# Kernel optimization log

Hardware: AMD Instinct MI355X
Metric: run time of the kernel (lower is better)

## Reference

```python
import jax, jax.numpy as jnp
import numpy as np

DIM = 512
HEADS = 8
HEAD_DIM = DIM // HEADS // 2  # 32
KS = 7  # kernel_size
DIL = 1


def _window_and_pb_start(length, ks):
    nh = ks // 2
    i = jnp.arange(length)
    ni = jnp.clip(i - nh, 0, length - ks)                       # neighborhood start
    pi = nh + jnp.maximum(nh - i, 0) + jnp.where(i + nh >= length, length - i - 1 - nh, 0)
    return ni, pi


def na_attention(qkv_na, rpb):
    # qkv_na: [B,H,W,3*heads*hd]
    B, H, W, _ = qkv_na.shape
    qkv = qkv_na.reshape(B, H, W, 3, HEADS, HEAD_DIM)
    qkv = jnp.transpose(qkv, (3, 0, 4, 1, 2, 5))                 # [3,B,h,H,W,d]
    q, k, v = qkv[0], qkv[1], qkv[2]
    scale = HEAD_DIM ** -0.5
    ni, pi = _window_and_pb_start(H, KS)
    nj, pj = _window_and_pb_start(W, KS)
    off = jnp.arange(KS)
    idx_i = ni[:, None] + off[None, :]                           # [H,K]
    idx_j = nj[:, None] + off[None, :]                           # [W,K]
    # gather neighborhoods: [B,h,H,W,K,K,d]
    kn = k[:, :, idx_i[:, None, :, None], idx_j[None, :, None, :], :]
    vn = v[:, :, idx_i[:, None, :, None], idx_j[None, :, None, :], :]
    bias_i = pi[:, None] + off[None, :]                          # [H,K]
    bias_j = pj[:, None] + off[None, :]                          # [W,K]
    bias = rpb[:, bias_i[:, None, :, None], bias_j[None, :, None, :]]  # [h,H,W,K,K]
    attn = jnp.einsum('bhijd,bhijkld->bhijkl', q * scale, kn) + bias[None]
    a = attn.reshape(B, HEADS, H, W, KS * KS)
    a = jax.nn.softmax(a, axis=-1).reshape(B, HEADS, H, W, KS, KS)
    out = jnp.einsum('bhijkl,bhijkld->bhijd', a, vn)             # [B,h,H,W,d]
    return jnp.transpose(out, (0, 2, 3, 1, 4)).reshape(B, H, W, HEADS * HEAD_DIM)


def self_attention(qkv_self):
    # qkv_self: [B,H,W,3*heads*hd]
    B, H, W, _ = qkv_self.shape
    N = H * W
    qkv = qkv_self.reshape(B, N, 3, HEADS, HEAD_DIM)
    qkv = jnp.transpose(qkv, (2, 0, 3, 1, 4))                    # [3,B,h,N,d]
    q, k, v = qkv[0], qkv[1], qkv[2]
    scale = HEAD_DIM ** -0.5
    scores = jnp.einsum('bhnd,bhmd->bhnm', q * scale, k)
    a = jax.nn.softmax(scores, axis=-1)
    out = jnp.einsum('bhnm,bhmd->bhnd', a, v)
    out = jnp.transpose(out, (0, 2, 1, 3)).reshape(B, H, W, HEADS * HEAD_DIM)
    return out


def setup_inputs() -> dict:
    key = jax.random.key(0)
    ks = jax.random.split(key, 6)
    B, H, W = 2, 48, 48
    x = jax.random.normal(ks[0], (B, H, W, DIM), dtype=jnp.float32)
    W_qkv = jax.random.normal(ks[1], (DIM, 3 * DIM), dtype=jnp.float32) * (DIM ** -0.5)
    b_qkv = jax.random.normal(ks[2], (3 * DIM,), dtype=jnp.float32) * 0.02
    rpb = jax.random.normal(ks[3], (HEADS, 2 * KS - 1, 2 * KS - 1), dtype=jnp.float32) * 0.02
    W_proj = jax.random.normal(ks[4], (DIM, DIM), dtype=jnp.float32) * (DIM ** -0.5)
    b_proj = jax.random.normal(ks[5], (DIM,), dtype=jnp.float32) * 0.02
    return {"x": x, "W_qkv": W_qkv, "b_qkv": b_qkv, "rpb": rpb, "W_proj": W_proj, "b_proj": b_proj}


def reference(x, W_qkv, b_qkv, rpb, W_proj, b_proj):
    B, H, W, C = x.shape
    qkv = x @ W_qkv + b_qkv                                      # [B,H,W,3C]
    qkv_na, qkv_self = qkv[..., : 3 * C // 2], qkv[..., 3 * C // 2:]
    x_na = na_attention(qkv_na, rpb)                             # [B,H,W,C//2]
    x_self = self_attention(qkv_self)                            # [B,H,W,C//2]
    out = jnp.concatenate([x_na, x_self], axis=-1) @ W_proj + b_proj
    return out
```

## Files before the change

kernel.cpp:

```cpp
#include <hip/hip_runtime.h>
#include <cstdint>
#include <cstddef>


#define DIMC 512
#define HEADS 8
#define HD 32
#define KSZ 7
#define HH 48
#define WW 48
#define BB 2
#define NPIX (HH * WW)
#define ROWS (BB * NPIX)
#define C3 (3 * DIMC)
#define TK 64
#define KSPLIT 4
#define KCHUNK (NPIX / KSPLIT)
#define NTILES (KCHUNK / TK)
#define QB 128
#define NQBLK (NPIX / QB)
#define NFLASH (16 * NQBLK * KSPLIT)
#define ROWE 40
#define VSTR 72
#define VROWE 232
#define LOG2E 1.4426950408889634f

typedef __attribute__((ext_vector_type(8))) short short8;
typedef __attribute__((ext_vector_type(4))) float f32x4;
union frag8 { short8 s; uint32_t u[4]; };

static __device__ __forceinline__ float bf2f(uint32_t u) {
    return __builtin_bit_cast(float, u << 16);
}
static __device__ __forceinline__ uint16_t f2bf(float f) {
    uint32_t x = __builtin_bit_cast(uint32_t, f);
    uint32_t r = x + 0x7fffu + ((x >> 16) & 1u);
    return (uint16_t)(r >> 16);
}
static __device__ __forceinline__ uint32_t cvtpk(float lo, float hi) {
    uint32_t r;
    asm("v_cvt_pk_bf16_f32 %0, %1, %2" : "=v"(r) : "v"(lo), "v"(hi));
    return r;
}
static __device__ __forceinline__ float ex2(float x) {
    return __builtin_amdgcn_exp2f(x);
}

__global__ __launch_bounds__(256)
void prep_weights(const float* __restrict__ Wqkv, const float* __restrict__ Wproj,
                  uint16_t* __restrict__ wqt, uint16_t* __restrict__ wpt)
{
    __shared__ float tile[32][33];
    int bid = blockIdx.x;
    const float* W; uint16_t* Wt; int N;
    if (bid < 768) { W = Wqkv; Wt = wqt; N = C3; }
    else { bid -= 768; W = Wproj; Wt = wpt; N = DIMC; }
    const int kt = bid & 15, nt = bid >> 4;
    const int K = DIMC;
    const int tx = threadIdx.x & 31, ty = threadIdx.x >> 5;
    const int k0 = kt * 32, n0 = nt * 32;
    #pragma unroll
    for (int i = 0; i < 4; ++i)
        tile[ty + 8 * i][tx] = W[(size_t)(k0 + ty + 8 * i) * N + n0 + tx];
    __syncthreads();
    #pragma unroll
    for (int i = 0; i < 4; ++i)
        Wt[(size_t)(n0 + ty + 8 * i) * K + k0 + tx] = f2bf(tile[tx][ty + 8 * i]);
}

template<bool A_F32, bool OUT_F32, bool QSCALE>
__global__ __launch_bounds__(256)
void gemm_mfma(const void* __restrict__ Av, const uint16_t* __restrict__ Bt,
               const float* __restrict__ bias, void* __restrict__ Cv,
               int M, int N, int K)
{
    constexpr int BM = 128, BK = 32;
    constexpr float QSC = 0.17677669529663687f * LOG2E;
    __shared__ __align__(16) uint16_t Al[BM * ROWE];
    __shared__ __align__(16) uint16_t Bl[BM * ROWE];
    const int tid = threadIdx.x;
    const int lane = tid & 63, wv = tid >> 6;
    const int c = lane & 15, g = lane >> 4;
    const int wr = wv >> 1, wc = wv & 1;
    const int m0 = blockIdx.y * BM, n0 = blockIdx.x * BM;
    const int srow = tid >> 2, skc = (tid & 3) * 8;

    f32x4 acc[4][4];
    #pragma unroll
    for (int mi = 0; mi < 4; ++mi)
        #pragma unroll
        for (int ni = 0; ni < 4; ++ni)
            acc[mi][ni] = (f32x4){0.f, 0.f, 0.f, 0.f};

    for (int k0 = 0; k0 < K; k0 += BK) {
        __syncthreads();
        #pragma unroll
        for (int half = 0; half < 2; ++half) {
            const int row = srow + half * 64;
            if (A_F32) {
                const float* A32 = (const float*)Av;
                const float4 a0 = *reinterpret_cast<const float4*>(&A32[(size_t)(m0 + row) * K + k0 + skc]);
                const float4 a1 = *reinterpret_cast<const float4*>(&A32[(size_t)(m0 + row) * K + k0 + skc + 4]);
                *reinterpret_cast<uint4*>(&Al[row * ROWE + skc]) =
                    make_uint4(cvtpk(a0.x, a0.y), cvtpk(a0.z, a0.w),
                               cvtpk(a1.x, a1.y), cvtpk(a1.z, a1.w));
            } else {
                const uint16_t* A16 = (const uint16_t*)Av;
                *reinterpret_cast<uint4*>(&Al[row * ROWE + skc]) =
                    *reinterpret_cast<const uint4*>(&A16[(size_t)(m0 + row) * K + k0 + skc]);
            }
            *reinterpret_cast<uint4*>(&Bl[row * ROWE + skc]) =
                *reinterpret_cast<const uint4*>(&Bt[(size_t)(n0 + row) * K + k0 + skc]);
        }
        __syncthreads();

        frag8 a[4], b[4];
        #pragma unroll
        for (int mi = 0; mi < 4; ++mi)
            a[mi].s = *reinterpret_cast<const short8*>(&Al[(wr * 64 + mi * 16 + c) * ROWE + g * 8]);
        #pragma unroll
        for (int ni = 0; ni < 4; ++ni)
            b[ni].s = *reinterpret_cast<const short8*>(&Bl[(wc * 64 + ni * 16 + c) * ROWE + g * 8]);
        #pragma unroll
        for (int mi = 0; mi < 4; ++mi)
            #pragma unroll
            for (int ni = 0; ni < 4; ++ni)
                acc[mi][ni] = __builtin_amdgcn_mfma_f32_16x16x32_bf16(
                    a[mi].s, b[ni].s, acc[mi][ni], 0, 0, 0);
    }

    #pragma unroll
    for (int mi = 0; mi < 4; ++mi) {
        #pragma unroll
        for (int ni = 0; ni < 4; ++ni) {
            const int row = m0 + wr * 64 + mi * 16 + 4 * g;
            const int col = n0 + wc * 64 + ni * 16 + c;
            const float bv = bias[col];
            float f = 1.f;
            if (QSCALE) f = (col < 256 || (col >= 768 && col < 1024)) ? QSC : 1.f;
            #pragma unroll
            for (int r = 0; r < 4; ++r) {
                const float val = (acc[mi][ni][r] + bv) * f;
                if (OUT_F32)
                    ((float*)Cv)[(size_t)(row + r) * N + col] = val;
                else
                    ((uint16_t*)Cv)[(size_t)(row + r) * N + col] = f2bf(val);
            }
        }
    }
}

static __device__ __forceinline__
void na_body(uint8_t* smem, int bid, const uint16_t* __restrict__ qkv,
             const float* __restrict__ rpb, uint16_t* __restrict__ attn)
{
    uint16_t* K_l   = (uint16_t*)smem;
    uint16_t* Vt    = (uint16_t*)(smem + 17920);
    float*    rpb_l = (float*)(smem + 32768);

    const int tid = threadIdx.x;
    const int lane = tid & 63, wv = tid >> 6;
    const int c = lane & 15, g = lane >> 4, g4 = g * 4;
    const int tile = bid % 36;
    const int bh = bid / 36;
    const int h = bh & (HEADS - 1), b = bh >> 3;
    const int t0i = (tile / 6) * 8, t0j = (tile % 6) * 8;
    const int u0i = min(max(t0i - 3, 0), HH - 14);
    const int u0j = min(max(t0j - 3, 0), WW - 14);
    const size_t rowbase = (size_t)b * NPIX;

    if (tid < 169) rpb_l[tid] = rpb[h * 169 + tid] * LOG2E;
    #pragma unroll
    for (int it = 0; it < 4; ++it) {
        const int idx = it * 256 + tid;
        if (idx < 896) {
            const int u = idx >> 2, dc = idx & 3;
            const int uc = u & 15, ur = u >> 4;
            if (uc < 14) {
                const int grow = (u0i + ur) * WW + (u0j + uc);
                const uint16_t* src = qkv + (rowbase + grow) * C3 + 256 + h * HD + dc * 8;
                *reinterpret_cast<uint4*>(&K_l[u * ROWE + dc * 8]) =
                    *reinterpret_cast<const uint4*>(src);
                const uint4 vw = *reinterpret_cast<const uint4*>(src + 256);
                const uint16_t* vh = reinterpret_cast<const uint16_t*>(&vw);
                #pragma unroll
                for (int i = 0; i < 8; ++i)
                    Vt[(dc * 8 + i) * VROWE + u] = vh[i];
            } else {
                *reinterpret_cast<uint4*>(&K_l[u * ROWE + dc * 8]) = make_uint4(0, 0, 0, 0);
                #pragma unroll
                for (int i = 0; i < 8; ++i)
                    Vt[(dc * 8 + i) * VROWE + u] = 0;
            }
        }
    }

    const int qid = wv * 16 + c;
    const int qi = t0i + (qid >> 3), qj = t0j + (qid & 7);
    const int pixq = qi * WW + qj;
    const int niq = min(max(qi - 3, 0), HH - KSZ);
    const int njq = min(max(qj - 3, 0), WW - KSZ);
    const int piq = 3 + max(3 - qi, 0) + ((qi + 3 >= HH) ? (HH - qi - 4) : 0);
    const int pjq = 3 + max(3 - qj, 0) + ((qj + 3 >= WW) ? (WW - qj - 4) : 0);
    const int ni_rel = niq - u0i, nj_rel = njq - u0j;
    const int bb = (piq - ni_rel) * 13 + (pjq - nj_rel);

    frag8 qf;
    qf.s = *reinterpret_cast<const short8*>(qkv + (rowbase + pixq) * C3 + h * HD + g * 8);

    __syncthreads();

    float pex[14][4];
    float m = -1e30f;
    #pragma unroll
    for (int f = 0; f < 14; ++f) {
        frag8 ka;
        ka.s = *reinterpret_cast<const short8*>(&K_l[(16 * f + c) * ROWE + g * 8]);
        f32x4 s = {0.f, 0.f, 0.f, 0.f};
        s = __builtin_amdgcn_mfma_f32_16x16x32_bf16(ka.s, qf.s, s, 0, 0, 0);
        const bool rok = (unsigned)(f - ni_rel) < 7u;
        #pragma unroll
        for (int r = 0; r < 4; ++r) {
            const int uc = g4 + r;
            const bool ok = rok && ((unsigned)(uc - nj_rel) < 7u);
            const int addr = ok ? (bb + 13 * f + uc) : 0;
            const float v = s[r] + rpb_l[addr];
            pex[f][r] = ok ? v : -1e30f;
            m = fmaxf(m, pex[f][r]);
        }
    }
    m = fmaxf(m, __shfl_xor(m, 16));
    m = fmaxf(m, __shfl_xor(m, 32));
    float l = 0.f;
    #pragma unroll
    for (int f = 0; f < 14; ++f)
        #pragma unroll
        for (int r = 0; r < 4; ++r) {
            pex[f][r] = ex2(pex[f][r] - m);
            l += pex[f][r];
        }
    l += __shfl_xor(l, 16);
    l += __shfl_xor(l, 32);

    f32x4 of0 = {0.f, 0.f, 0.f, 0.f}, of1 = {0.f, 0.f, 0.f, 0.f};
    const int sbase = (g & 1) * 32 + c;
    #pragma unroll
    for (int kk = 0; kk < 7; ++kk) {
        uint32_t pk0[2], pk1[2];
        pk0[0] = cvtpk(pex[2 * kk][0], pex[2 * kk][1]);
        pk0[1] = cvtpk(pex[2 * kk][2], pex[2 * kk][3]);
        pk1[0] = cvtpk(pex[2 * kk + 1][0], pex[2 * kk + 1][1]);
        pk1[1] = cvtpk(pex[2 * kk + 1][2], pex[2 * kk + 1][3]);
        frag8 pb;
        #pragma unroll
        for (int tt = 0; tt < 4; ++tt) {
            const int srcLane = sbase + ((tt >> 1) << 4);
            const uint32_t v0 = __shfl(pk0[tt & 1], srcLane);
            const uint32_t v1 = __shfl(pk1[tt & 1], srcLane);
            pb.u[tt] = (g >= 2) ? v1 : v0;
        }
        frag8 va0, va1;
        va0.s = *reinterpret_cast<const short8*>(&Vt[c * VROWE + kk * 32 + g * 8]);
        va1.s = *reinterpret_cast<const short8*>(&Vt[(16 + c) * VROWE + kk * 32 + g * 8]);
        of0 = __builtin_amdgcn_mfma_f32_16x16x32_bf16(va0.s, pb.s, of0, 0, 0, 0);
        of1 = __builtin_amdgcn_mfma_f32_16x16x32_bf16(va1.s, pb.s, of1, 0, 0, 0);
    }

    const float invl = 1.f / l;
    uint32_t* dst = reinterpret_cast<uint32_t*>(attn + (rowbase + pixq) * DIMC + h * HD);
    dst[2 * g + 0] = cvtpk(of0[0] * invl, of0[1] * invl);
    dst[2 * g + 1] = cvtpk(of0[2] * invl, of0[3] * invl);
    dst[8 + 2 * g + 0] = cvtpk(of1[0] * invl, of1[1] * invl);
    dst[8 + 2 * g + 1] = cvtpk(of1[2] * invl, of1[3] * invl);
}

static __device__ __forceinline__
void flash_body(uint8_t* smem, int bid, const uint16_t* __restrict__ qkv,
                uint16_t* __restrict__ po, float2* __restrict__ pml)
{
    uint16_t (*Ks)[TK * ROWE]  = (uint16_t (*)[TK * ROWE])smem;
    uint16_t (*Vt)[32 * VSTR]  = (uint16_t (*)[32 * VSTR])(smem + 10240);

    const int tid = threadIdx.x;
    const int lane = tid & 63, wv = tid >> 6;
    const int c = lane & 15, g = lane >> 4;
    const int split = bid & (KSPLIT - 1);
    const int qblk = (bid >> 2) % NQBLK;
    const int bh = bid / (KSPLIT * NQBLK);
    const int h = bh & (HEADS - 1);
    const int b = bh >> 3;
    const size_t rowbase = (size_t)b * NPIX;
    const int qbase = qblk * QB + wv * 32;
    const int q0 = qbase + c, q1 = qbase + 16 + c;

    frag8 qf0, qf1;
    qf0.s = *reinterpret_cast<const short8*>(qkv + (rowbase + q0) * C3 + 768 + h * HD + g * 8);
    qf1.s = *reinterpret_cast<const short8*>(qkv + (rowbase + q1) * C3 + 768 + h * HD + g * 8);

    float m0 = -1e30f, m1 = -1e30f, ls0 = 0.f, ls1 = 0.f;
    f32x4 oa00 = {0,0,0,0}, oa01 = {0,0,0,0};
    f32x4 oa10 = {0,0,0,0}, oa11 = {0,0,0,0};

    const int skk = tid >> 2, kd = (tid & 3) * 8;
    const int sgk = (skk & 15) | ((skk & 16) << 1) | ((skk & 32) >> 1);
    const int skv = tid >> 3, sdc = tid & 7;
    const int cp2 = 2 * (skv ^ ((sdc >> 1) << 3));

    uint4 KW; uint2 VA, VB;
#define STAGE_LOAD(T) do {                                                            \
    const size_t _tb = rowbase + split * KCHUNK + (T) * TK;                           \
    KW = *reinterpret_cast<const uint4*>(qkv + (_tb + sgk) * C3 + 1024 + h * HD + kd);\
    const uint16_t* _vp = qkv + (_tb + skv) * C3 + 1280 + h * HD + sdc * 4;           \
    VA = *reinterpret_cast<const uint2*>(_vp);                                        \
    VB = *reinterpret_cast<const uint2*>(_vp + 32 * C3); } while (0)

#define STAGE_WRITE(BUF) do {                                                         \
    *reinterpret_cast<uint4*>(&Ks[BUF][skk * ROWE + kd]) = KW;                        \
    const uint32_t _pa[4] = {VA.x & 0xffffu, VA.x >> 16, VA.y & 0xffffu, VA.y >> 16}; \
    const uint32_t _pb[4] = {VB.x & 0xffffu, VB.x >> 16, VB.y & 0xffffu, VB.y >> 16}; \
    _Pragma("unroll")                                                                 \
    for (int _i = 0; _i < 4; ++_i)                                                    \
        *reinterpret_cast<uint32_t*>(&Vt[BUF][(sdc * 4 + _i) * VSTR + cp2]) =         \
            _pa[_i] | (_pb[_i] << 16); } while (0)

    STAGE_LOAD(0);
    STAGE_WRITE(0);

    const int x0 = (c >> 3) << 3;
    const int x1 = 16 + x0;

    for (int t = 0; t < NTILES; ++t) {
        __syncthreads();

        const bool more = (t + 1 < NTILES);
        if (more) STAGE_LOAD(t + 1);

        const int cur = t & 1;
        frag8 ka0, ka1, ka2, ka3;
        ka0.s = *reinterpret_cast<const short8*>(&Ks[cur][c * ROWE + g * 8]);
        ka1.s = *reinterpret_cast<const short8*>(&Ks[cur][(16 + c) * ROWE + g * 8]);
        ka2.s = *reinterpret_cast<const short8*>(&Ks[cur][(32 + c) * ROWE + g * 8]);
        ka3.s = *reinterpret_cast<const short8*>(&Ks[cur][(48 + c) * ROWE + g * 8]);
        f32x4 sc0[4], sc1[4];
        #pragma unroll
        for (int kf = 0; kf < 4; ++kf) {
            sc0[kf] = (f32x4){0,0,0,0};
            sc1[kf] = (f32x4){0,0,0,0};
        }
        __builtin_amdgcn_s_setprio(1);
        sc0[0] = __builtin_amdgcn_mfma_f32_16x16x32_bf16(ka0.s, qf0.s, sc0[0], 0, 0, 0);
        sc0[1] = __builtin_amdgcn_mfma_f32_16x16x32_bf16(ka1.s, qf0.s, sc0[1], 0, 0, 0);
        sc0[2] = __builtin_amdgcn_mfma_f32_16x16x32_bf16(ka2.s, qf0.s, sc0[2], 0, 0, 0);
        sc0[3] = __builtin_amdgcn_mfma_f32_16x16x32_bf16(ka3.s, qf0.s, sc0[3], 0, 0, 0);
        sc1[0] = __builtin_amdgcn_mfma_f32_16x16x32_bf16(ka0.s, qf1.s, sc1[0], 0, 0, 0);
        sc1[1] = __builtin_amdgcn_mfma_f32_16x16x32_bf16(ka1.s, qf1.s, sc1[1], 0, 0, 0);
        sc1[2] = __builtin_amdgcn_mfma_f32_16x16x32_bf16(ka2.s, qf1.s, sc1[2], 0, 0, 0);
        sc1[3] = __builtin_amdgcn_mfma_f32_16x16x32_bf16(ka3.s, qf1.s, sc1[3], 0, 0, 0);
        __builtin_amdgcn_s_setprio(0);

        float t0 = sc0[0][0], t1 = sc1[0][0];
        #pragma unroll
        for (int kf = 0; kf < 4; ++kf)
            #pragma unroll
            for (int r = 0; r < 4; ++r) {
                t0 = fmaxf(t0, sc0[kf][r]);
                t1 = fmaxf(t1, sc1[kf][r]);
            }
        t0 = fmaxf(t0, __shfl_xor(t0, 16)); t0 = fmaxf(t0, __shfl_xor(t0, 32));
        t1 = fmaxf(t1, __shfl_xor(t1, 16)); t1 = fmaxf(t1, __shfl_xor(t1, 32));

        const int ok = (t0 - m0 <= 11.54f) && (t1 - m1 <= 11.54f);
        if (!__all(ok)) {
            const float nm0 = fmaxf(m0, t0), nm1 = fmaxf(m1, t1);
            const float c0 = ex2(m0 - nm0), c1 = ex2(m1 - nm1);
            ls0 *= c0; ls1 *= c1;
            oa00 *= c0; oa01 *= c0; oa10 *= c1; oa11 *= c1;
            m0 = nm0; m1 = nm1;
        }

        #pragma unroll
        for (int kf = 0; kf < 4; ++kf)
            #pragma unroll
            for (int r = 0; r < 4; ++r) {
                sc0[kf][r] = ex2(sc0[kf][r] - m0); ls0 += sc0[kf][r];
                sc1[kf][r] = ex2(sc1[kf][r] - m1); ls1 += sc1[kf][r];
            }

        #pragma unroll
        for (int kk = 0; kk < 2; ++kk) {
            frag8 pb0, pb1;
            #pragma unroll
            for (int tt = 0; tt < 4; ++tt) {
                pb0.u[tt] = cvtpk(sc0[2 * kk][tt], sc0[2 * kk + 1][tt]);
                pb1.u[tt] = cvtpk(sc1[2 * kk][tt], sc1[2 * kk + 1][tt]);
            }
            const int p0 = 16 * kk + 4 * g;
            frag8 va0, va1;
            va0.s = *reinterpret_cast<const short8*>(&Vt[cur][c * VSTR + 2 * (p0 ^ x0)]);
            va1.s = *reinterpret_cast<const short8*>(&Vt[cur][(16 + c) * VSTR + 2 * (p0 ^ x1)]);
            __builtin_amdgcn_s_setprio(1);
            oa00 = __builtin_amdgcn_mfma_f32_16x16x32_bf16(va0.s, pb0.s, oa00, 0, 0, 0);
            oa01 = __builtin_amdgcn_mfma_f32_16x16x32_bf16(va1.s, pb0.s, oa01, 0, 0, 0);
            oa10 = __builtin_amdgcn_mfma_f32_16x16x32_bf16(va0.s, pb1.s, oa10, 0, 0, 0);
            oa11 = __builtin_amdgcn_mfma_f32_16x16x32_bf16(va1.s, pb1.s, oa11, 0, 0, 0);
            __builtin_amdgcn_s_setprio(0);
        }

        if (more) STAGE_WRITE(cur ^ 1);
    }

    ls0 += __shfl_xor(ls0, 16); ls0 += __shfl_xor(ls0, 32);
    ls1 += __shfl_xor(ls1, 16); ls1 += __shfl_xor(ls1, 32);

    const float i0 = 1.f / ls0, i1 = 1.f / ls1;
    const size_t item0 = ((size_t)split * 16 + bh) * NPIX + q0;
    const size_t item1 = ((size_t)split * 16 + bh) * NPIX + q1;
    uint32_t* d0 = reinterpret_cast<uint32_t*>(po + item0 * HD);
    d0[2 * g + 0] = cvtpk(oa00[0] * i0, oa00[1] * i0);
    d0[2 * g + 1] = cvtpk(oa00[2] * i0, oa00[3] * i0);
    d0[8 + 2 * g + 0] = cvtpk(oa01[0] * i0, oa01[1] * i0);
    d0[8 + 2 * g + 1] = cvtpk(oa01[2] * i0, oa01[3] * i0);
    uint32_t* d1 = reinterpret_cast<uint32_t*>(po + item1 * HD);
    d1[2 * g + 0] = cvtpk(oa10[0] * i1, oa10[1] * i1);
    d1[2 * g + 1] = cvtpk(oa10[2] * i1, oa10[3] * i1);
    d1[8 + 2 * g + 0] = cvtpk(oa11[0] * i1, oa11[1] * i1);
    d1[8 + 2 * g + 1] = cvtpk(oa11[2] * i1, oa11[3] * i1);
    if (g == 0) {
        pml[item0] = make_float2(m0, ls0);
        pml[item1] = make_float2(m1, ls1);
    }
#undef STAGE_LOAD
#undef STAGE_WRITE
}

__global__ __launch_bounds__(256)
void attn_fused(const uint16_t* __restrict__ qkv, const float* __restrict__ rpb,
                uint16_t* __restrict__ attn, uint16_t* __restrict__ po,
                float2* __restrict__ pml)
{
    __shared__ __align__(16) uint8_t smem[33456];
    const int bid = blockIdx.x;
    if (bid < NFLASH)
        flash_body(smem, bid, qkv, po, pml);
    else
        na_body(smem, bid - NFLASH, qkv, rpb, attn);
}

__global__ __launch_bounds__(256)
void self_attn_combine(const uint16_t* __restrict__ po, const float2* __restrict__ pml,
                       uint16_t* __restrict__ attn)
{
    const int idx = blockIdx.x * 256 + threadIdx.x;
    const int d = idx & (HD - 1);
    const int q = (idx >> 5) % NPIX;
    const int bh = idx / (HD * NPIX);
    const int h = bh & (HEADS - 1);
    const int b = bh >> 3;

    float2 ml[KSPLIT];
    float M = -1e30f;
    #pragma unroll
    for (int s = 0; s < KSPLIT; ++s) {
        ml[s] = pml[((size_t)s * 16 + bh) * NPIX + q];
        M = fmaxf(M, ml[s].x);
    }
    float num = 0.f, den = 0.f;
    #pragma unroll
    for (int s = 0; s < KSPLIT; ++s) {
        const float w = ex2(ml[s].x - M) * ml[s].y;
        const float o = bf2f((uint32_t)po[(((size_t)s * 16 + bh) * NPIX + q) * HD + d]);
        num = fmaf(w, o, num);
        den += w;
    }
    attn[((size_t)b * NPIX + q) * DIMC + 256 + h * HD + d] = f2bf(num / den);
}

extern "C" void kernel_launch(void* const* d_in, const int* in_sizes, int n_in,
                              void* d_out, int out_size, void* d_ws, size_t ws_size,
                              hipStream_t stream)
{
    const float* x     = (const float*)d_in[0];
    const float* Wqkv  = (const float*)d_in[1];
    const float* bqkv  = (const float*)d_in[2];
    const float* rpb   = (const float*)d_in[3];
    const float* Wproj = (const float*)d_in[4];
    const float* bproj = (const float*)d_in[5];

    uint16_t* qkv  = (uint16_t*)d_ws;
    uint16_t* attn = qkv + (size_t)ROWS * C3;
    uint16_t* wqt  = attn + (size_t)ROWS * DIMC;
    uint16_t* wpt  = wqt + (size_t)C3 * DIMC;
    uint16_t* po   = wpt + (size_t)DIMC * DIMC;
    float2*   pml  = (float2*)(po + (size_t)KSPLIT * 16 * NPIX * HD);

    const dim3 blk(256);
    prep_weights<<<dim3(1024), blk, 0, stream>>>(Wqkv, Wproj, wqt, wpt);
    gemm_mfma<true, false, true><<<dim3(C3 / 128, ROWS / 128), blk, 0, stream>>>(
        x, wqt, bqkv, qkv, ROWS, C3, DIMC);
    attn_fused<<<dim3(NFLASH + BB * HEADS * 36), blk, 0, stream>>>(qkv, rpb, attn, po, pml);
    self_attn_combine<<<dim3((16 * NPIX * HD) / 256), blk, 0, stream>>>(po, pml, attn);
    gemm_mfma<false, true, false><<<dim3(DIMC / 128, ROWS / 128), blk, 0, stream>>>(
        attn, wpt, bproj, d_out, ROWS, DIMC, DIMC);
}
```

Baseline: 81.90 us.

## Fuse split-K flash combine into attention kernel via last-block atomic counter

Removes the separate self_attn_combine launch. Each flash split block now bumps a per-(head, query-block) atomic counter after writing its partial output and max/sum. The last split to arrive merges all KSPLIT partials and writes the final bf16 self-attention output, then resets the counter. This saves a kernel launch and a pass over global memory, at the cost of threadfences, an atomic per block, and a serial merge tail in whichever block finishes last.

```diff
diff --git a/kernel.cpp b/kernel.cpp
--- a/kernel.cpp
+++ b/kernel.cpp
@@ -20,10 +20,13 @@
 #define QB 128
 #define NQBLK (NPIX / QB)
 #define NFLASH (16 * NQBLK * KSPLIT)
+#define NNA (BB * HEADS * 36)
+#define NGRP (16 * NQBLK)
 #define ROWE 40
 #define VSTR 72
 #define VROWE 232
 #define LOG2E 1.4426950408889634f
+#define SMEM_BYTES 33456
 
 typedef __attribute__((ext_vector_type(8))) short short8;
 typedef __attribute__((ext_vector_type(4))) float f32x4;
@@ -48,10 +51,14 @@
 
 __global__ __launch_bounds__(256)
 void prep_weights(const float* __restrict__ Wqkv, const float* __restrict__ Wproj,
-                  uint16_t* __restrict__ wqt, uint16_t* __restrict__ wpt)
+                  uint16_t* __restrict__ wqt, uint16_t* __restrict__ wpt,
+                  int* __restrict__ cnt)
 {
     __shared__ float tile[32][33];
     int bid = blockIdx.x;
+    if (bid == 0) {
+        for (int i = threadIdx.x; i < NGRP; i += 256) cnt[i] = 0;
+    }
     const float* W; uint16_t* Wt; int N;
     if (bid < 768) { W = Wqkv; Wt = wqt; N = C3; }
     else { bid -= 768; W = Wproj; Wt = wpt; N = DIMC; }
@@ -276,7 +283,8 @@
 
 static __device__ __forceinline__
 void flash_body(uint8_t* smem, int bid, const uint16_t* __restrict__ qkv,
-                uint16_t* __restrict__ po, float2* __restrict__ pml)
+                uint16_t* __restrict__ po, float2* __restrict__ pml,
+                uint16_t* __restrict__ attn, int* __restrict__ cnt)
 {
     uint16_t (*Ks)[TK * ROWE]  = (uint16_t (*)[TK * ROWE])smem;
     uint16_t (*Vt)[32 * VSTR]  = (uint16_t (*)[32 * VSTR])(smem + 10240);
@@ -429,6 +437,61 @@
         pml[item0] = make_float2(m0, ls0);
         pml[item1] = make_float2(m1, ls1);
     }
+
+    __syncthreads();
+    volatile int* flag = (volatile int*)smem;
+    __threadfence();
+    if (tid == 0) {
+        const int grp = bh * NQBLK + qblk;
+        *flag = atomicAdd(&cnt[grp], 1);
+    }
+    __syncthreads();
+    if (*flag == KSPLIT - 1) {
+        __threadfence();
+        const int ql = tid >> 1;
+        const int d0c = (tid & 1) * 16;
+        const int q = qblk * QB + ql;
+        float2 mlv[KSPLIT];
+        float M2 = -1e30f;
+        #pragma unroll
+        for (int s = 0; s < KSPLIT; ++s) {
+            mlv[s] = pml[((size_t)(s * 16 + bh)) * NPIX + q];
+            M2 = fmaxf(M2, mlv[s].x);
+        }
+        float ws_[KSPLIT], den = 0.f;
+        #pragma unroll
+        for (int s = 0; s < KSPLIT; ++s) {
+            ws_[s] = ex2(mlv[s].x - M2) * mlv[s].y;
+            den += ws_[s];
+        }
+        const float inv = 1.f / den;
+        float accv[16] = {};
+        #pragma unroll
+        for (int s = 0; s < KSPLIT; ++s) {
+            const uint16_t* src = po + (((size_t)(s * 16 + bh)) * NPIX + q) * HD + d0c;
+            #pragma unroll
+            for (int half = 0; half < 2; ++half) {
+                const uint4 wq = *reinterpret_cast<const uint4*>(src + half * 8);
+                const uint32_t wd[4] = {wq.x, wq.y, wq.z, wq.w};
+                #pragma unroll
+                for (int jp = 0; jp < 4; ++jp) {
+                    accv[half * 8 + 2 * jp + 0] = fmaf(ws_[s], bf2f(wd[jp] & 0xffffu),
+                                                       accv[half * 8 + 2 * jp + 0]);
+                    accv[half * 8 + 2 * jp + 1] = fmaf(ws_[s], bf2f(wd[jp] >> 16),
+                                                       accv[half * 8 + 2 * jp + 1]);
+                }
+            }
+        }
+        uint32_t outw[8];
+        #pragma unroll
+        for (int jp = 0; jp < 8; ++jp)
+            outw[jp] = cvtpk(accv[2 * jp] * inv, accv[2 * jp + 1] * inv);
+        uint32_t* dst = reinterpret_cast<uint32_t*>(
+            attn + (rowbase + q) * DIMC + 256 + h * HD + d0c);
+        *reinterpret_cast<uint4*>(dst)     = make_uint4(outw[0], outw[1], outw[2], outw[3]);
+        *reinterpret_cast<uint4*>(dst + 4) = make_uint4(outw[4], outw[5], outw[6], outw[7]);
+        if (tid == 0) cnt[bh * NQBLK + qblk] = 0;
+    }
 #undef STAGE_LOAD
 #undef STAGE_WRITE
 }
@@ -436,43 +499,14 @@
 __global__ __launch_bounds__(256)
 void attn_fused(const uint16_t* __restrict__ qkv, const float* __restrict__ rpb,
                 uint16_t* __restrict__ attn, uint16_t* __restrict__ po,
-                float2* __restrict__ pml)
+                float2* __restrict__ pml, int* __restrict__ cnt)
 {
-    __shared__ __align__(16) uint8_t smem[33456];
+    __shared__ __align__(16) uint8_t smem[SMEM_BYTES];
     const int bid = blockIdx.x;
     if (bid < NFLASH)
-        flash_body(smem, bid, qkv, po, pml);
+        flash_body(smem, bid, qkv, po, pml, attn, cnt);
     else
         na_body(smem, bid - NFLASH, qkv, rpb, attn);
-}
-
-__global__ __launch_bounds__(256)
-void self_attn_combine(const uint16_t* __restrict__ po, const float2* __restrict__ pml,
-                       uint16_t* __restrict__ attn)
-{
-    const int idx = blockIdx.x * 256 + threadIdx.x;
-    const int d = idx & (HD - 1);
-    const int q = (idx >> 5) % NPIX;
-    const int bh = idx / (HD * NPIX);
-    const int h = bh & (HEADS - 1);
-    const int b = bh >> 3;
-
-    float2 ml[KSPLIT];
-    float M = -1e30f;
-    #pragma unroll
-    for (int s = 0; s < KSPLIT; ++s) {
-        ml[s] = pml[((size_t)s * 16 + bh) * NPIX + q];
-        M = fmaxf(M, ml[s].x);
-    }
-    float num = 0.f, den = 0.f;
-    #pragma unroll
-    for (int s = 0; s < KSPLIT; ++s) {
-        const float w = ex2(ml[s].x - M) * ml[s].y;
-        const float o = bf2f((uint32_t)po[(((size_t)s * 16 + bh) * NPIX + q) * HD + d]);
-        num = fmaf(w, o, num);
-        den += w;
-    }
-    attn[((size_t)b * NPIX + q) * DIMC + 256 + h * HD + d] = f2bf(num / den);
 }
 
 extern "C" void kernel_launch(void* const* d_in, const int* in_sizes, int n_in,
@@ -492,13 +526,13 @@
     uint16_t* wpt  = wqt + (size_t)C3 * DIMC;
     uint16_t* po   = wpt + (size_t)DIMC * DIMC;
     float2*   pml  = (float2*)(po + (size_t)KSPLIT * 16 * NPIX * HD);
+    int*      cnt  = (int*)(pml + (size_t)KSPLIT * 16 * NPIX);
 
     const dim3 blk(256);
-    prep_weights<<<dim3(1024), blk, 0, stream>>>(Wqkv, Wproj, wqt, wpt);
+    prep_weights<<<dim3(1024), blk, 0, stream>>>(Wqkv, Wproj, wqt, wpt, cnt);
     gemm_mfma<true, false, true><<<dim3(C3 / 128, ROWS / 128), blk, 0, stream>>>(
         x, wqt, bqkv, qkv, ROWS, C3, DIMC);
-    attn_fused<<<dim3(NFLASH + BB * HEADS * 36), blk, 0, stream>>>(qkv, rpb, attn, po, pml);
-    self_attn_combine<<<dim3((16 * NPIX * HD) / 256), blk, 0, stream>>>(po, pml, attn);
+    attn_fused<<<dim3(NFLASH + NNA), blk, 0, stream>>>(qkv, rpb, attn, po, pml, cnt);
     gemm_mfma<false, true, false><<<dim3(DIMC / 128, ROWS / 128), blk, 0, stream>>>(
-        attn, wpt, bproj, d_out, ROWS, DIMC, DIMC);
-}
+        attn, wpt, bproj, (float*)d_out, ROWS, DIMC, DIMC);
+}
```

Result: slower. 318.3 us (median of 2 runs) (+288.7%).

## Alias V tile over K in shared memory to shrink attention LDS footprint

Applied to the files above, without the earlier changes.

The neighborhood-attention body now loads the transposed V tile only after the QK/softmax phase. It places V in the same shared-memory region as K, with barriers on both sides, and moves the relative-position-bias table to sit just after that region. This cuts the fused attention kernel's static LDS allocation from about 33 KB to about 19 KB, so more blocks of both flash and NA work can be resident per CU. The cost is that the V global loads can no longer overlap with the K loads, plus two extra barriers. The change is only safe if the flash body also fits in the smaller buffer.

```diff
diff --git a/kernel.cpp b/kernel.cpp
--- a/kernel.cpp
+++ b/kernel.cpp
@@ -20,10 +20,12 @@
 #define QB 128
 #define NQBLK (NPIX / QB)
 #define NFLASH (16 * NQBLK * KSPLIT)
+#define NNA (BB * HEADS * 36)
 #define ROWE 40
 #define VSTR 72
 #define VROWE 232
 #define LOG2E 1.4426950408889634f
+#define SMEM_BYTES 19456
 
 typedef __attribute__((ext_vector_type(8))) short short8;
 typedef __attribute__((ext_vector_type(4))) float f32x4;
@@ -155,8 +157,8 @@
              const float* __restrict__ rpb, uint16_t* __restrict__ attn)
 {
     uint16_t* K_l   = (uint16_t*)smem;
-    uint16_t* Vt    = (uint16_t*)(smem + 17920);
-    float*    rpb_l = (float*)(smem + 32768);
+    float*    rpb_l = (float*)(smem + 17920);
+    uint16_t* Vt    = (uint16_t*)smem;
 
     const int tid = threadIdx.x;
     const int lane = tid & 63, wv = tid >> 6;
@@ -178,19 +180,11 @@
             const int uc = u & 15, ur = u >> 4;
             if (uc < 14) {
                 const int grow = (u0i + ur) * WW + (u0j + uc);
-                const uint16_t* src = qkv + (rowbase + grow) * C3 + 256 + h * HD + dc * 8;
                 *reinterpret_cast<uint4*>(&K_l[u * ROWE + dc * 8]) =
-                    *reinterpret_cast<const uint4*>(src);
-                const uint4 vw = *reinterpret_cast<const uint4*>(src + 256);
-                const uint16_t* vh = reinterpret_cast<const uint16_t*>(&vw);
-                #pragma unroll
-                for (int i = 0; i < 8; ++i)
-                    Vt[(dc * 8 + i) * VROWE + u] = vh[i];
+                    *reinterpret_cast<const uint4*>(
+                        qkv + (rowbase + grow) * C3 + 256 + h * HD + dc * 8);
             } else {
                 *reinterpret_cast<uint4*>(&K_l[u * ROWE + dc * 8]) = make_uint4(0, 0, 0, 0);
-                #pragma unroll
-                for (int i = 0; i < 8; ++i)
-                    Vt[(dc * 8 + i) * VROWE + u] = 0;
             }
         }
     }
@@ -241,6 +235,30 @@
         }
     l += __shfl_xor(l, 16);
     l += __shfl_xor(l, 32);
+
+    __syncthreads();
+    #pragma unroll
+    for (int it = 0; it < 4; ++it) {
+        const int idx = it * 256 + tid;
+        if (idx < 896) {
+            const int u = idx >> 2, dc = idx & 3;
+            const int uc = u & 15, ur = u >> 4;
+            if (uc < 14) {
+                const int grow = (u0i + ur) * WW + (u0j + uc);
+                const uint4 vw = *reinterpret_cast<const uint4*>(
+                    qkv + (rowbase + grow) * C3 + 512 + h * HD + dc * 8);
+                const uint16_t* vh = reinterpret_cast<const uint16_t*>(&vw);
+                #pragma unroll
+                for (int i = 0; i < 8; ++i)
+                    Vt[(dc * 8 + i) * VROWE + u] = vh[i];
+            } else {
+                #pragma unroll
+                for (int i = 0; i < 8; ++i)
+                    Vt[(dc * 8 + i) * VROWE + u] = 0;
+            }
+        }
+    }
+    __syncthreads();
 
     f32x4 of0 = {0.f, 0.f, 0.f, 0.f}, of1 = {0.f, 0.f, 0.f, 0.f};
     const int sbase = (g & 1) * 32 + c;
@@ -438,7 +456,7 @@
                 uint16_t* __restrict__ attn, uint16_t* __restrict__ po,
                 float2* __restrict__ pml)
 {
-    __shared__ __align__(16) uint8_t smem[33456];
+    __shared__ __align__(16) uint8_t smem[SMEM_BYTES];
     const int bid = blockIdx.x;
     if (bid < NFLASH)
         flash_body(smem, bid, qkv, po, pml);
@@ -497,8 +515,8 @@
     prep_weights<<<dim3(1024), blk, 0, stream>>>(Wqkv, Wproj, wqt, wpt);
     gemm_mfma<true, false, true><<<dim3(C3 / 128, ROWS / 128), blk, 0, stream>>>(
         x, wqt, bqkv, qkv, ROWS, C3, DIMC);
-    attn_fused<<<dim3(NFLASH + BB * HEADS * 36), blk, 0, stream>>>(qkv, rpb, attn, po, pml);
+    attn_fused<<<dim3(NFLASH + NNA), blk, 0, stream>>>(qkv, rpb, attn, po, pml);
     self_attn_combine<<<dim3((16 * NPIX * HD) / 256), blk, 0, stream>>>(po, pml, attn);
     gemm_mfma<false, true, false><<<dim3(DIMC / 128, ROWS / 128), blk, 0, stream>>>(
-        attn, wpt, bproj, d_out, ROWS, DIMC, DIMC);
-}
+        attn, wpt, bproj, (float*)d_out, ROWS, DIMC, DIMC);
+}
```

New measurement: 83.16 us. No clear change (+1.5%).
